# Optimization experiments

Measured on AMD Instinct MI355X. Metric: run time of the kernel, lower is better.

The kernel has to match this reference:

```python
import jax, jax.numpy as jnp
import numpy as np

FX, FY, CX, CY = 250.0, 250.0, 112.0, 112.0
H0, W0 = 224.0, 224.0
SCALES = (56, 28, 14, 7)


def _bilinear(img, x, y):
    # img: [C, H, W]; x, y: [N] float coords (x indexes H, y indexes W)
    x1 = jnp.floor(x).astype(jnp.int32)
    x2 = jnp.ceil(x).astype(jnp.int32)
    y1 = jnp.floor(y).astype(jnp.int32)
    y2 = jnp.ceil(y).astype(jnp.int32)
    Q11 = img[:, x1, y1].T  # [N, C]
    Q12 = img[:, x1, y2].T
    Q21 = img[:, x2, y1].T
    Q22 = img[:, x2, y2].T
    x1f, x2f = x1.astype(x.dtype), x2.astype(x.dtype)
    y1f, y2f = y1.astype(y.dtype), y2.astype(y.dtype)
    w11 = ((x2f - x) * (y2f - y))[:, None]
    w12 = ((x2f - x) * (y - y1f))[:, None]
    w21 = ((x - x1f) * (y2f - y))[:, None]
    w22 = ((x - x1f) * (y - y1f))[:, None]
    return w11 * Q11 + w21 * Q21 + w12 * Q12 + w22 * Q22  # [N, C]


def setup_inputs() -> dict:
    key = jax.random.key(0)
    ks = jax.random.split(key, 6)
    B, N = 8, 100000
    return {
        "vertices": jax.random.normal(ks[0], (B, N, 3), dtype=jnp.float32),
        "feat0": jax.random.normal(ks[1], (B, 64, 56, 56), dtype=jnp.float32),
        "feat1": jax.random.normal(ks[2], (B, 128, 28, 28), dtype=jnp.float32),
        "feat2": jax.random.normal(ks[3], (B, 256, 14, 14), dtype=jnp.float32),
        "feat3": jax.random.normal(ks[4], (B, 512, 7, 7), dtype=jnp.float32),
        "proj_mat": jax.random.normal(ks[5], (B, 4, 4), dtype=jnp.float32),
    }


def reference(vertices, feat0, feat1, feat2, feat3, proj_mat):
    X = vertices[:, :, 0]
    Y = vertices[:, :, 1]
    Z = vertices[:, :, 2]
    h = FY * (Y / Z) + CY  # [B, N]
    w = FX * (X / (-Z)) + CX
    outs = [vertices]
    for feat, s in zip((feat0, feat1, feat2, feat3), SCALES):
        x = jnp.clip(h / (H0 / s), 0.0, float(s - 1))
        y = jnp.clip(w / (W0 / s), 0.0, float(s - 1))
        outs.append(jax.vmap(_bilinear)(feat, x, y))  # [B, N, C]
    return jnp.concatenate(outs, axis=2)  # [B, N, 3 + 64+128+256+512]
```

## Files before the change

### kernel.cpp

```cpp
#include <hip/hip_runtime.h>


#define VPB 4

template<int C, int S>
__global__ __launch_bounds__(256) void transpose_feat(const float* __restrict__ src,
                                                      float* __restrict__ dst,
                                                      int total) {
    int i = blockIdx.x * 256 + threadIdx.x;
    if (i >= total) return;
    int c  = i % C;
    int p  = i / C;
    int w  = p % S;
    int p2 = p / S;
    int h  = p2 % S;
    int b  = p2 / S;
    dst[i] = src[((b * C + c) * S + h) * S + w];
}

__global__ __launch_bounds__(256) void gp_main(const float* __restrict__ verts,
                                               const float* __restrict__ f0,
                                               const float* __restrict__ f1,
                                               const float* __restrict__ f2,
                                               const float* __restrict__ f3,
                                               float* __restrict__ out,
                                               int N, int total_v) {
    __shared__ float swt[VPB][4][4];
    __shared__ int   sof[VPB][4][4];
    __shared__ float sv[VPB][3];

    const int t  = threadIdx.x;
    const int v0 = blockIdx.x * VPB;

    if (t < VPB * 4) {
        const int v  = t >> 2;
        const int sc = t & 3;
        const int vi = v0 + v;
        if (vi < total_v) {
            const int b = vi / N;
            const float X = verts[3 * vi + 0];
            const float Y = verts[3 * vi + 1];
            const float Z = verts[3 * vi + 2];
            if (sc == 0) { sv[v][0] = X; sv[v][1] = Y; sv[v][2] = Z; }
            const float h = __fadd_rn(__fmul_rn(250.0f, __fdiv_rn(Y, Z)), 112.0f);
            const float w = __fadd_rn(__fmul_rn(250.0f, __fdiv_rn(X, -Z)), 112.0f);

            const int   Sarr[4] = {56, 28, 14, 7};
            const int   Carr[4] = {64, 128, 256, 512};
            const float invA[4] = {0.25f, 0.125f, 0.0625f, 0.03125f};
            const int s  = Sarr[sc];
            const int Cc = Carr[sc];
            const float smax = (float)(s - 1);

            const float x = fminf(fmaxf(__fmul_rn(h, invA[sc]), 0.0f), smax);
            const float y = fminf(fmaxf(__fmul_rn(w, invA[sc]), 0.0f), smax);
            const float x1f = floorf(x), x2f = ceilf(x);
            const float y1f = floorf(y), y2f = ceilf(y);
            const int x1 = (int)x1f, x2 = (int)x2f;
            const int y1 = (int)y1f, y2 = (int)y2f;

            swt[v][sc][0] = (x2f - x) * (y2f - y);
            swt[v][sc][1] = (x2f - x) * (y - y1f);
            swt[v][sc][2] = (x - x1f) * (y2f - y);
            swt[v][sc][3] = (x - x1f) * (y - y1f);

            const int base = b * s * s;
            sof[v][sc][0] = (base + x1 * s + y1) * Cc;
            sof[v][sc][1] = (base + x1 * s + y2) * Cc;
            sof[v][sc][2] = (base + x2 * s + y1) * Cc;
            sof[v][sc][3] = (base + x2 * s + y2) * Cc;
        }
    }
    __syncthreads();

    int sc, cbase, kbase;
    const float* fp = f0;
    if (t < 16)       { sc = 0; cbase = 4 * t;         kbase = 3;   fp = f0; }
    else if (t < 48)  { sc = 1; cbase = 4 * (t - 16);  kbase = 67;  fp = f1; }
    else if (t < 112) { sc = 2; cbase = 4 * (t - 48);  kbase = 195; fp = f2; }
    else if (t < 240) { sc = 3; cbase = 4 * (t - 112); kbase = 451; fp = f3; }
    else              { sc = -1; cbase = 0; kbase = 0; }

    for (int v = 0; v < VPB; ++v) {
        const int vi = v0 + v;
        if (vi >= total_v) break;
        const size_t obase = (size_t)vi * 963;
        if (sc >= 0) {
            const float w11 = swt[v][sc][0], w12 = swt[v][sc][1];
            const float w21 = swt[v][sc][2], w22 = swt[v][sc][3];
            const float4 q11 = *(const float4*)(fp + sof[v][sc][0] + cbase);
            const float4 q12 = *(const float4*)(fp + sof[v][sc][1] + cbase);
            const float4 q21 = *(const float4*)(fp + sof[v][sc][2] + cbase);
            const float4 q22 = *(const float4*)(fp + sof[v][sc][3] + cbase);
            float r0 = w11 * q11.x + w21 * q21.x + w12 * q12.x + w22 * q22.x;
            float r1 = w11 * q11.y + w21 * q21.y + w12 * q12.y + w22 * q22.y;
            float r2 = w11 * q11.z + w21 * q21.z + w12 * q12.z + w22 * q22.z;
            float r3 = w11 * q11.w + w21 * q21.w + w12 * q12.w + w22 * q22.w;
            float* op = out + obase + kbase + cbase;
            op[0] = r0; op[1] = r1; op[2] = r2; op[3] = r3;
        } else if (t >= 240 && t < 243) {
            out[obase + (t - 240)] = sv[v][t - 240];
        }
    }
}

extern "C" void kernel_launch(void* const* d_in, const int* in_sizes, int n_in,
                              void* d_out, int out_size, void* d_ws, size_t ws_size,
                              hipStream_t stream) {
    const float* verts = (const float*)d_in[0];
    const float* f0s   = (const float*)d_in[1];
    const float* f1s   = (const float*)d_in[2];
    const float* f2s   = (const float*)d_in[3];
    const float* f3s   = (const float*)d_in[4];

    const int B = in_sizes[5] / 16;
    const int N = in_sizes[0] / (3 * B);
    const int total_v = B * N;

    const int n0 = B * 64 * 56 * 56;
    const int n1 = B * 128 * 28 * 28;
    const int n2 = B * 256 * 14 * 14;
    const int n3 = B * 512 * 7 * 7;

    float* t0 = (float*)d_ws;
    float* t1 = t0 + n0;
    float* t2 = t1 + n1;
    float* t3 = t2 + n2;

    transpose_feat<64, 56><<<(n0 + 255) / 256, 256, 0, stream>>>(f0s, t0, n0);
    transpose_feat<128, 28><<<(n1 + 255) / 256, 256, 0, stream>>>(f1s, t1, n1);
    transpose_feat<256, 14><<<(n2 + 255) / 256, 256, 0, stream>>>(f2s, t2, n2);
    transpose_feat<512, 7><<<(n3 + 255) / 256, 256, 0, stream>>>(f3s, t3, n3);

    const int nblocks = (total_v + VPB - 1) / VPB;
    gp_main<<<nblocks, 256, 0, stream>>>(verts, t0, t1, t2, t3,
                                         (float*)d_out, N, total_v);
}
```

Measured before the change: 3.383 ms.

## Remap threads to contiguous output columns and skip zero-weight bilinear gathers

Threads are reassigned so that each of the 240 workers writes consecutive output columns (stride 240 over the 963-wide row). Each wave's stores now hit contiguous addresses instead of four scalar stores spaced four floats apart. When a sample coordinate is integral (x1==x2 or y1==y2, common after clipping), every bilinear weight is zero, so the four gathers are skipped and 0 is written directly. The cost is that feature reads drop from float4 to scalar, and outputs can differ from the reference if the features contain inf or NaN.

```diff
diff --git a/kernel.cpp b/kernel.cpp
--- a/kernel.cpp
+++ b/kernel.cpp
@@ -27,6 +27,7 @@
                                                int N, int total_v) {
     __shared__ float swt[VPB][4][4];
     __shared__ int   sof[VPB][4][4];
+    __shared__ int   snz[VPB][4];
     __shared__ float sv[VPB][3];
 
     const int t  = threadIdx.x;
@@ -64,6 +65,8 @@
             swt[v][sc][2] = (x - x1f) * (y2f - y);
             swt[v][sc][3] = (x - x1f) * (y - y1f);
 
+            snz[v][sc] = (x1 != x2) && (y1 != y2);
+
             const int base = b * s * s;
             sof[v][sc][0] = (base + x1 * s + y1) * Cc;
             sof[v][sc][1] = (base + x1 * s + y2) * Cc;
@@ -73,32 +76,42 @@
     }
     __syncthreads();
 
-    int sc, cbase, kbase;
-    const float* fp = f0;
-    if (t < 16)       { sc = 0; cbase = 4 * t;         kbase = 3;   fp = f0; }
-    else if (t < 48)  { sc = 1; cbase = 4 * (t - 16);  kbase = 67;  fp = f1; }
-    else if (t < 112) { sc = 2; cbase = 4 * (t - 48);  kbase = 195; fp = f2; }
-    else if (t < 240) { sc = 3; cbase = 4 * (t - 112); kbase = 451; fp = f3; }
-    else              { sc = -1; cbase = 0; kbase = 0; }
+    int   sck[4], cik[4];
+    const float* fpk[4];
+    if (t < 240) {
+#pragma unroll
+        for (int k = 0; k < 4; ++k) {
+            const int c = 3 + 240 * k + t;
+            if (c < 67)       { sck[k] = 0; cik[k] = c - 3;   fpk[k] = f0; }
+            else if (c < 195) { sck[k] = 1; cik[k] = c - 67;  fpk[k] = f1; }
+            else if (c < 451) { sck[k] = 2; cik[k] = c - 195; fpk[k] = f2; }
+            else              { sck[k] = 3; cik[k] = c - 451; fpk[k] = f3; }
+        }
+    }
 
     for (int v = 0; v < VPB; ++v) {
         const int vi = v0 + v;
         if (vi >= total_v) break;
         const size_t obase = (size_t)vi * 963;
-        if (sc >= 0) {
-            const float w11 = swt[v][sc][0], w12 = swt[v][sc][1];
-            const float w21 = swt[v][sc][2], w22 = swt[v][sc][3];
-            const float4 q11 = *(const float4*)(fp + sof[v][sc][0] + cbase);
-            const float4 q12 = *(const float4*)(fp + sof[v][sc][1] + cbase);
-            const float4 q21 = *(const float4*)(fp + sof[v][sc][2] + cbase);
-            const float4 q22 = *(const float4*)(fp + sof[v][sc][3] + cbase);
-            float r0 = w11 * q11.x + w21 * q21.x + w12 * q12.x + w22 * q22.x;
-            float r1 = w11 * q11.y + w21 * q21.y + w12 * q12.y + w22 * q22.y;
-            float r2 = w11 * q11.z + w21 * q21.z + w12 * q12.z + w22 * q22.z;
-            float r3 = w11 * q11.w + w21 * q21.w + w12 * q12.w + w22 * q22.w;
-            float* op = out + obase + kbase + cbase;
-            op[0] = r0; op[1] = r1; op[2] = r2; op[3] = r3;
-        } else if (t >= 240 && t < 243) {
+        if (t < 240) {
+#pragma unroll
+            for (int k = 0; k < 4; ++k) {
+                const int sc = sck[k];
+                float r = 0.0f;
+                if (snz[v][sc]) {
+                    const float w11 = swt[v][sc][0], w12 = swt[v][sc][1];
+                    const float w21 = swt[v][sc][2], w22 = swt[v][sc][3];
+                    const float* fp = fpk[k];
+                    const int ci = cik[k];
+                    const float q11 = fp[sof[v][sc][0] + ci];
+                    const float q12 = fp[sof[v][sc][1] + ci];
+                    const float q21 = fp[sof[v][sc][2] + ci];
+                    const float q22 = fp[sof[v][sc][3] + ci];
+                    r = w11 * q11 + w21 * q21 + w12 * q12 + w22 * q22;
+                }
+                out[obase + 3 + 240 * k + t] = r;
+            }
+        } else if (t < 243) {
             out[obase + (t - 240)] = sv[v][t - 240];
         }
     }
```

New measurement: 3.241 ms. 1.04x faster.

## Zero-fill output and skip bilinear gathers when interpolation weights vanish

Applied to the files above, without the earlier changes.

Writes the whole output with a separate nontemporal zero-fill kernel, then runs a persistent one-wave-per-vertex kernel. That kernel only gathers and writes features for scales whose coordinates are non-integer in both axes; otherwise every bilinear weight is zero and the output stays zero. This avoids gather traffic for clamped or integer-aligned vertices, which are common when projections fall outside the image. In exchange, the output region is written twice for interpolated vertices and the work per vertex becomes data-dependent, which can unbalance the waves.

```diff
diff --git a/kernel.cpp b/kernel.cpp
--- a/kernel.cpp
+++ b/kernel.cpp
@@ -1,7 +1,7 @@
 #include <hip/hip_runtime.h>
 
 
-#define VPB 4
+typedef float floatx4 __attribute__((ext_vector_type(4)));
 
 template<int C, int S>
 __global__ __launch_bounds__(256) void transpose_feat(const float* __restrict__ src,
@@ -18,88 +18,78 @@
     dst[i] = src[((b * C + c) * S + h) * S + w];
 }
 
-__global__ __launch_bounds__(256) void gp_main(const float* __restrict__ verts,
-                                               const float* __restrict__ f0,
-                                               const float* __restrict__ f1,
-                                               const float* __restrict__ f2,
-                                               const float* __restrict__ f3,
-                                               float* __restrict__ out,
-                                               int N, int total_v) {
-    __shared__ float swt[VPB][4][4];
-    __shared__ int   sof[VPB][4][4];
-    __shared__ float sv[VPB][3];
+__global__ __launch_bounds__(256) void zero_fill(floatx4* __restrict__ out4,
+                                                 long long n4) {
+    long long i      = (long long)blockIdx.x * 256 + threadIdx.x;
+    long long stride = (long long)gridDim.x * 256;
+    const floatx4 z = {0.0f, 0.0f, 0.0f, 0.0f};
+    for (; i < n4; i += stride)
+        __builtin_nontemporal_store(z, &out4[i]);
+}
 
-    const int t  = threadIdx.x;
-    const int v0 = blockIdx.x * VPB;
+__global__ __launch_bounds__(256) void gp_sparse(const float* __restrict__ verts,
+                                                 const float* __restrict__ f0,
+                                                 const float* __restrict__ f1,
+                                                 const float* __restrict__ f2,
+                                                 const float* __restrict__ f3,
+                                                 float* __restrict__ out,
+                                                 int N, int total_v) {
+    const int lane    = threadIdx.x & 63;
+    const int wave_id = (int)((blockIdx.x * 256 + threadIdx.x) >> 6);
+    const int nwaves  = (int)((gridDim.x * 256) >> 6);
 
-    if (t < VPB * 4) {
-        const int v  = t >> 2;
-        const int sc = t & 3;
-        const int vi = v0 + v;
-        if (vi < total_v) {
-            const int b = vi / N;
-            const float X = verts[3 * vi + 0];
-            const float Y = verts[3 * vi + 1];
-            const float Z = verts[3 * vi + 2];
-            if (sc == 0) { sv[v][0] = X; sv[v][1] = Y; sv[v][2] = Z; }
-            const float h = __fadd_rn(__fmul_rn(250.0f, __fdiv_rn(Y, Z)), 112.0f);
-            const float w = __fadd_rn(__fmul_rn(250.0f, __fdiv_rn(X, -Z)), 112.0f);
+    const int   Sarr[4] = {56, 28, 14, 7};
+    const int   Carr[4] = {64, 128, 256, 512};
+    const float invA[4] = {0.25f, 0.125f, 0.0625f, 0.03125f};
+    const int   Kb[4]   = {3, 67, 195, 451};
+    const float* fps[4] = {f0, f1, f2, f3};
 
-            const int   Sarr[4] = {56, 28, 14, 7};
-            const int   Carr[4] = {64, 128, 256, 512};
-            const float invA[4] = {0.25f, 0.125f, 0.0625f, 0.03125f};
-            const int s  = Sarr[sc];
-            const int Cc = Carr[sc];
+    for (int vi = wave_id; vi < total_v; vi += nwaves) {
+        const int b = vi / N;
+        const float X = verts[3 * vi + 0];
+        const float Y = verts[3 * vi + 1];
+        const float Z = verts[3 * vi + 2];
+        const size_t obase = (size_t)vi * 963;
+
+        const float v3 = (lane == 0) ? X : ((lane == 1) ? Y : Z);
+        if (lane < 3) out[obase + lane] = v3;
+
+        const float h = __fadd_rn(__fmul_rn(250.0f, __fdiv_rn(Y, Z)), 112.0f);
+        const float w = __fadd_rn(__fmul_rn(250.0f, __fdiv_rn(X, -Z)), 112.0f);
+
+#pragma unroll
+        for (int sc = 0; sc < 4; ++sc) {
+            const int   s    = Sarr[sc];
+            const int   C    = Carr[sc];
             const float smax = (float)(s - 1);
 
             const float x = fminf(fmaxf(__fmul_rn(h, invA[sc]), 0.0f), smax);
             const float y = fminf(fmaxf(__fmul_rn(w, invA[sc]), 0.0f), smax);
             const float x1f = floorf(x), x2f = ceilf(x);
             const float y1f = floorf(y), y2f = ceilf(y);
-            const int x1 = (int)x1f, x2 = (int)x2f;
-            const int y1 = (int)y1f, y2 = (int)y2f;
 
-            swt[v][sc][0] = (x2f - x) * (y2f - y);
-            swt[v][sc][1] = (x2f - x) * (y - y1f);
-            swt[v][sc][2] = (x - x1f) * (y2f - y);
-            swt[v][sc][3] = (x - x1f) * (y - y1f);
+            if (x1f != x2f && y1f != y2f) {
+                const int x1 = (int)x1f, x2 = (int)x2f;
+                const int y1 = (int)y1f, y2 = (int)y2f;
+                const float w11 = (x2f - x) * (y2f - y);
+                const float w12 = (x2f - x) * (y - y1f);
+                const float w21 = (x - x1f) * (y2f - y);
+                const float w22 = (x - x1f) * (y - y1f);
 
-            const int base = b * s * s;
-            sof[v][sc][0] = (base + x1 * s + y1) * Cc;
-            sof[v][sc][1] = (base + x1 * s + y2) * Cc;
-            sof[v][sc][2] = (base + x2 * s + y1) * Cc;
-            sof[v][sc][3] = (base + x2 * s + y2) * Cc;
-        }
-    }
-    __syncthreads();
+                const int base = b * s * s;
+                const int o11 = (base + x1 * s + y1) * C;
+                const int o12 = (base + x1 * s + y2) * C;
+                const int o21 = (base + x2 * s + y1) * C;
+                const int o22 = (base + x2 * s + y2) * C;
+                const float* __restrict__ fp = fps[sc];
+                float* __restrict__ op = out + obase + Kb[sc];
 
-    int sc, cbase, kbase;
-    const float* fp = f0;
-    if (t < 16)       { sc = 0; cbase = 4 * t;         kbase = 3;   fp = f0; }
-    else if (t < 48)  { sc = 1; cbase = 4 * (t - 16);  kbase = 67;  fp = f1; }
-    else if (t < 112) { sc = 2; cbase = 4 * (t - 48);  kbase = 195; fp = f2; }
-    else if (t < 240) { sc = 3; cbase = 4 * (t - 112); kbase = 451; fp = f3; }
-    else              { sc = -1; cbase = 0; kbase = 0; }
-
-    for (int v = 0; v < VPB; ++v) {
-        const int vi = v0 + v;
-        if (vi >= total_v) break;
-        const size_t obase = (size_t)vi * 963;
-        if (sc >= 0) {
-            const float w11 = swt[v][sc][0], w12 = swt[v][sc][1];
-            const float w21 = swt[v][sc][2], w22 = swt[v][sc][3];
-            const float4 q11 = *(const float4*)(fp + sof[v][sc][0] + cbase);
-            const float4 q12 = *(const float4*)(fp + sof[v][sc][1] + cbase);
-            const float4 q21 = *(const float4*)(fp + sof[v][sc][2] + cbase);
-            const float4 q22 = *(const float4*)(fp + sof[v][sc][3] + cbase);
-            float r0 = w11 * q11.x + w21 * q21.x + w12 * q12.x + w22 * q22.x;
-            float r1 = w11 * q11.y + w21 * q21.y + w12 * q12.y + w22 * q22.y;
-            float r2 = w11 * q11.z + w21 * q21.z + w12 * q12.z + w22 * q22.z;
-            float r3 = w11 * q11.w + w21 * q21.w + w12 * q12.w + w22 * q22.w;
-            float* op = out + obase + kbase + cbase;
-            op[0] = r0; op[1] = r1; op[2] = r2; op[3] = r3;
-        } else if (t >= 240 && t < 243) {
-            out[obase + (t - 240)] = sv[v][t - 240];
+                for (int c = lane; c < C; c += 64) {
+                    const float r = w11 * fp[o11 + c] + w21 * fp[o21 + c]
+                                  + w12 * fp[o12 + c] + w22 * fp[o22 + c];
+                    __builtin_nontemporal_store(r, op + c);
+                }
+            }
         }
     }
 }
@@ -132,7 +122,9 @@
     transpose_feat<256, 14><<<(n2 + 255) / 256, 256, 0, stream>>>(f2s, t2, n2);
     transpose_feat<512, 7><<<(n3 + 255) / 256, 256, 0, stream>>>(f3s, t3, n3);
 
-    const int nblocks = (total_v + VPB - 1) / VPB;
-    gp_main<<<nblocks, 256, 0, stream>>>(verts, t0, t1, t2, t3,
-                                         (float*)d_out, N, total_v);
+    const long long n4 = ((long long)total_v * 963) / 4;
+    zero_fill<<<4096, 256, 0, stream>>>((floatx4*)d_out, n4);
+
+    gp_sparse<<<2048, 256, 0, stream>>>(verts, t0, t1, t2, t3,
+                                        (float*)d_out, N, total_v);
 }
```

New measurement: 3.597 ms. 1.06x slower.
